# Kernel tuning notes

Hardware: AMD Instinct MI355X
Metric: run time of the kernel (lower is better)

The kernel has to match this reference:

```python
import jax, jax.numpy as jnp
import numpy as np

GROUP, BS, CH = 16, 8192, 256


def setup_inputs() -> dict:
    key = jax.random.key(0)
    kx, kw = jax.random.split(key)
    x = jax.random.normal(kx, (GROUP, BS, CH), dtype=jnp.float32)
    # PyTorch init: uniform(-stdv, stdv), stdv = 1/sqrt(channels)
    stdv = 1.0 / np.sqrt(CH)
    weight = jax.random.uniform(kw, (GROUP, CH, CH), dtype=jnp.float32,
                                minval=-stdv, maxval=stdv)
    return {"x": x, "weight": weight}


def reference(x, weight):
    # x: (group, bs, n); weight: (group, n, channels). For each column i of
    # weight (w: (group, n)) apply Householder-style reflection sequentially:
    #   x <- x - (2 / (w^T w)) * (x @ w) w^T
    ws = jnp.moveaxis(weight, -1, 0)  # (channels, group, n)

    def step(xc, w):
        denom = jnp.sum(w * w, axis=-1)              # (group,)
        xw = jnp.einsum('gbn,gn->gb', xc, w)         # (group, bs)
        xc = xc - (2.0 / denom)[:, None, None] * xw[..., None] * w[:, None, :]
        return xc, None

    out, _ = jax.lax.scan(step, x, ws)
    return out
```

## Files before the change

### kernel.cpp

```cpp
#include <hip/hip_runtime.h>
#include <hip/hip_bf16.h>

#define GROUPS 16
#define BSZ    8192
#define CHN    256

using f32x4  = __attribute__((ext_vector_type(4))) float;
using bf16x8 = __attribute__((ext_vector_type(8))) __bf16;

static __device__ __forceinline__ unsigned short f32_bf16(float f) {
    unsigned int u = __builtin_bit_cast(unsigned int, f);
    u = (u + 0x7FFFu + ((u >> 16) & 1u)) >> 16;
    return (unsigned short)u;
}
static __device__ __forceinline__ unsigned int pack_bf16x2(float lo, float hi) {
    return (unsigned int)f32_bf16(lo) | ((unsigned int)f32_bf16(hi) << 16);
}

__global__ __launch_bounds__(256) void compose_m(const float* __restrict__ weight,
                                                 unsigned short* __restrict__ Mt) {
    __shared__ float wbuf[16 * 260];
    __shared__ float coefbuf[16];

    const int t    = threadIdx.x;
    const int g    = blockIdx.x >> 4;
    const int r0   = (blockIdx.x & 15) * 16;
    const int lane = t & 15;
    const int rg   = (t >> 4) & 3;
    const int wave = t >> 6;
    const int r    = r0 + wave * 4 + rg;

    float4 m4[4];
#pragma unroll
    for (int j = 0; j < 4; ++j) {
        const int cb = 4 * lane + 64 * j;
        m4[j].x = (cb + 0 == r) ? 1.0f : 0.0f;
        m4[j].y = (cb + 1 == r) ? 1.0f : 0.0f;
        m4[j].z = (cb + 2 == r) ? 1.0f : 0.0f;
        m4[j].w = (cb + 3 == r) ? 1.0f : 0.0f;
    }

    const float* wg = weight + (size_t)g * CHN * CHN;
    const int e16 = t & 15;
    const int nb  = t >> 4;

    for (int iw = 0; iw < 16; ++iw) {
        const int i0 = iw * 16;
        float ld[16];
#pragma unroll
        for (int k = 0; k < 16; ++k)
            ld[k] = wg[(nb + 16 * k) * CHN + i0 + e16];
        __syncthreads();
#pragma unroll
        for (int k = 0; k < 16; ++k)
            wbuf[e16 * 260 + nb + 16 * k] = ld[k];
        __syncthreads();
        {
            const int e = t >> 4;
            float s = 0.0f;
#pragma unroll
            for (int k = 0; k < 16; ++k) {
                const float w = wbuf[e * 260 + lane + 16 * k];
                s += w * w;
            }
            s += __shfl_xor(s, 1);
            s += __shfl_xor(s, 2);
            s += __shfl_xor(s, 4);
            s += __shfl_xor(s, 8);
            if (lane == 0) coefbuf[e] = 2.0f / s;
        }
        __syncthreads();
#pragma unroll
        for (int e = 0; e < 16; ++e) {
            float4 w4[4];
#pragma unroll
            for (int j = 0; j < 4; ++j)
                w4[j] = *(const float4*)&wbuf[e * 260 + 4 * lane + 64 * j];
            float p = 0.0f;
#pragma unroll
            for (int j = 0; j < 4; ++j)
                p += m4[j].x * w4[j].x + m4[j].y * w4[j].y +
                     m4[j].z * w4[j].z + m4[j].w * w4[j].w;
            p += __shfl_xor(p, 1);
            p += __shfl_xor(p, 2);
            p += __shfl_xor(p, 4);
            p += __shfl_xor(p, 8);
            const float s = coefbuf[e] * p;
#pragma unroll
            for (int j = 0; j < 4; ++j) {
                m4[j].x -= s * w4[j].x;
                m4[j].y -= s * w4[j].y;
                m4[j].z -= s * w4[j].z;
                m4[j].w -= s * w4[j].w;
            }
        }
    }

    unsigned short* mg = Mt + (size_t)g * CHN * CHN;
#pragma unroll
    for (int j = 0; j < 4; ++j) {
        const int cb = 4 * lane + 64 * j;
        mg[(size_t)(cb + 0) * CHN + r] = f32_bf16(m4[j].x);
        mg[(size_t)(cb + 1) * CHN + r] = f32_bf16(m4[j].y);
        mg[(size_t)(cb + 2) * CHN + r] = f32_bf16(m4[j].z);
        mg[(size_t)(cb + 3) * CHN + r] = f32_bf16(m4[j].w);
    }
}

__global__ __launch_bounds__(512, 4) void gemm_xm(const float* __restrict__ x,
                                                  const unsigned short* __restrict__ Mt,
                                                  float* __restrict__ out) {
    __shared__ unsigned int xa [128 * 37];
    __shared__ unsigned int mts[256 * 37];

    const int t    = threadIdx.x;
    const int g    = blockIdx.x >> 6;
    const int rb   = blockIdx.x & 63;
    const int r0   = rb * 128;
    const int l    = t & 63;
    const int wave = t >> 6;
    const int wr   = wave >> 2;
    const int wc   = wave & 3;
    const int lm   = l & 15;
    const int q    = l >> 4;

    const float*          xg = x  + ((size_t)g * BSZ + r0) * CHN;
    const unsigned short* mg = Mt +  (size_t)g * CHN * CHN;

    f32x4 acc[4][4];
#pragma unroll
    for (int mi = 0; mi < 4; ++mi)
#pragma unroll
        for (int ni = 0; ni < 4; ++ni)
            acc[mi][ni] = (f32x4){0.f, 0.f, 0.f, 0.f};

    const int srr = t >> 4;
    const int sk4 = t & 15;
    const int mc  = t >> 1;
    const int mh  = t & 1;

    for (int kc = 0; kc < 4; ++kc) {
        const int k0 = kc * 64;
        __syncthreads();
#pragma unroll
        for (int it = 0; it < 4; ++it) {
            const int rr = srr + it * 32;
            const float4 v = *(const float4*)&xg[(size_t)rr * CHN + k0 + 4 * sk4];
            xa[rr * 37 + 2 * sk4 + 0] = pack_bf16x2(v.x, v.y);
            xa[rr * 37 + 2 * sk4 + 1] = pack_bf16x2(v.z, v.w);
        }
        {
            const uint4* src = (const uint4*)(mg + (size_t)mc * CHN + k0 + 32 * mh);
#pragma unroll
            for (int s = 0; s < 4; ++s) {
                const uint4 v = src[s];
                const int base = mc * 37 + 16 * mh + 4 * s;
                mts[base + 0] = v.x;
                mts[base + 1] = v.y;
                mts[base + 2] = v.z;
                mts[base + 3] = v.w;
            }
        }
        __syncthreads();
#pragma unroll
        for (int ks = 0; ks < 2; ++ks) {
            const int koff = 16 * ks + 4 * q;
            bf16x8 a[4], b[4];
#pragma unroll
            for (int mi = 0; mi < 4; ++mi) {
                const int rr = wr * 64 + mi * 16 + lm;
                uint4 u;
                u.x = xa[rr * 37 + koff + 0];
                u.y = xa[rr * 37 + koff + 1];
                u.z = xa[rr * 37 + koff + 2];
                u.w = xa[rr * 37 + koff + 3];
                a[mi] = __builtin_bit_cast(bf16x8, u);
            }
#pragma unroll
            for (int ni = 0; ni < 4; ++ni) {
                const int cc = wc * 64 + ni * 16 + lm;
                uint4 u;
                u.x = mts[cc * 37 + koff + 0];
                u.y = mts[cc * 37 + koff + 1];
                u.z = mts[cc * 37 + koff + 2];
                u.w = mts[cc * 37 + koff + 3];
                b[ni] = __builtin_bit_cast(bf16x8, u);
            }
#pragma unroll
            for (int mi = 0; mi < 4; ++mi)
#pragma unroll
                for (int ni = 0; ni < 4; ++ni)
                    acc[mi][ni] = __builtin_amdgcn_mfma_f32_16x16x32_bf16(
                        a[mi], b[ni], acc[mi][ni], 0, 0, 0);
        }
    }

    float* og = out + ((size_t)g * BSZ + r0) * CHN;
#pragma unroll
    for (int mi = 0; mi < 4; ++mi) {
#pragma unroll
        for (int ni = 0; ni < 4; ++ni) {
            const int col = wc * 64 + ni * 16 + lm;
#pragma unroll
            for (int reg = 0; reg < 4; ++reg) {
                const int row = wr * 64 + mi * 16 + q * 4 + reg;
                og[(size_t)row * CHN + col] = acc[mi][ni][reg];
            }
        }
    }
}

extern "C" void kernel_launch(void* const* d_in, const int* in_sizes, int n_in,
                              void* d_out, int out_size, void* d_ws, size_t ws_size,
                              hipStream_t stream) {
    const float* x = (const float*)d_in[0];
    const float* w = (const float*)d_in[1];
    float* out = (float*)d_out;
    unsigned short* Mt = (unsigned short*)d_ws;

    hipLaunchKernelGGL(compose_m, dim3(GROUPS * 16), dim3(256), 0, stream, w, Mt);
    hipLaunchKernelGGL(gemm_xm,   dim3(GROUPS * 64), dim3(512), 0, stream, x, Mt, out);
}
```

Measured before the change: 330.5 us.

## Replace LDS-tiled GEMM with register-streaming MFMA kernel and prefetch weights in compose

The GEMM kernel drops shared-memory staging and barriers. Each wave now owns 32 rows by all 256 columns and loads x and M fragments directly from global memory into MFMA operand registers. The compose kernel also prefetches the next weight chunk into registers before the reflection loop, and splits the dot-product reduction into four partial sums. The costs are heavy register pressure from 32 accumulators plus 16 B fragments, and redundant global reads of M across waves that now depend on the cache.

```diff
diff --git a/kernel.cpp b/kernel.cpp
--- a/kernel.cpp
+++ b/kernel.cpp
@@ -15,6 +15,14 @@
 }
 static __device__ __forceinline__ unsigned int pack_bf16x2(float lo, float hi) {
     return (unsigned int)f32_bf16(lo) | ((unsigned int)f32_bf16(hi) << 16);
+}
+static __device__ __forceinline__ bf16x8 pack8(float4 u, float4 v) {
+    uint4 d;
+    d.x = pack_bf16x2(u.x, u.y);
+    d.y = pack_bf16x2(u.z, u.w);
+    d.z = pack_bf16x2(v.x, v.y);
+    d.w = pack_bf16x2(v.z, v.w);
+    return __builtin_bit_cast(bf16x8, d);
 }
 
 __global__ __launch_bounds__(256) void compose_m(const float* __restrict__ weight,
@@ -44,17 +52,23 @@
     const int e16 = t & 15;
     const int nb  = t >> 4;
 
+    float ld[16];
+#pragma unroll
+    for (int k = 0; k < 16; ++k)
+        ld[k] = wg[(nb + 16 * k) * CHN + e16];
+
     for (int iw = 0; iw < 16; ++iw) {
-        const int i0 = iw * 16;
-        float ld[16];
-#pragma unroll
-        for (int k = 0; k < 16; ++k)
-            ld[k] = wg[(nb + 16 * k) * CHN + i0 + e16];
         __syncthreads();
 #pragma unroll
         for (int k = 0; k < 16; ++k)
             wbuf[e16 * 260 + nb + 16 * k] = ld[k];
         __syncthreads();
+        if (iw < 15) {
+            const int i0 = (iw + 1) * 16;
+#pragma unroll
+            for (int k = 0; k < 16; ++k)
+                ld[k] = wg[(nb + 16 * k) * CHN + i0 + e16];
+        }
         {
             const int e = t >> 4;
             float s = 0.0f;
@@ -76,11 +90,15 @@
 #pragma unroll
             for (int j = 0; j < 4; ++j)
                 w4[j] = *(const float4*)&wbuf[e * 260 + 4 * lane + 64 * j];
-            float p = 0.0f;
-#pragma unroll
-            for (int j = 0; j < 4; ++j)
-                p += m4[j].x * w4[j].x + m4[j].y * w4[j].y +
-                     m4[j].z * w4[j].z + m4[j].w * w4[j].w;
+            float p0 = m4[0].x * w4[0].x + m4[0].y * w4[0].y +
+                       m4[0].z * w4[0].z + m4[0].w * w4[0].w;
+            float p1 = m4[1].x * w4[1].x + m4[1].y * w4[1].y +
+                       m4[1].z * w4[1].z + m4[1].w * w4[1].w;
+            float p2 = m4[2].x * w4[2].x + m4[2].y * w4[2].y +
+                       m4[2].z * w4[2].z + m4[2].w * w4[2].w;
+            float p3 = m4[3].x * w4[3].x + m4[3].y * w4[3].y +
+                       m4[3].z * w4[3].z + m4[3].w * w4[3].w;
+            float p = (p0 + p1) + (p2 + p3);
             p += __shfl_xor(p, 1);
             p += __shfl_xor(p, 2);
             p += __shfl_xor(p, 4);
@@ -107,103 +125,62 @@
     }
 }
 
-__global__ __launch_bounds__(512, 4) void gemm_xm(const float* __restrict__ x,
-                                                  const unsigned short* __restrict__ Mt,
-                                                  float* __restrict__ out) {
-    __shared__ unsigned int xa [128 * 37];
-    __shared__ unsigned int mts[256 * 37];
-
+__global__ __launch_bounds__(256, 2) void gemm_stream(const float* __restrict__ x,
+                                                      const unsigned short* __restrict__ Mt,
+                                                      float* __restrict__ out) {
     const int t    = threadIdx.x;
+    const int wave = t >> 6;
+    const int l    = t & 63;
+    const int lm   = l & 15;
+    const int q    = l >> 4;
     const int g    = blockIdx.x >> 6;
     const int rb   = blockIdx.x & 63;
-    const int r0   = rb * 128;
-    const int l    = t & 63;
-    const int wave = t >> 6;
-    const int wr   = wave >> 2;
-    const int wc   = wave & 3;
-    const int lm   = l & 15;
-    const int q    = l >> 4;
+    const int r0   = rb * 128 + wave * 32;
 
     const float*          xg = x  + ((size_t)g * BSZ + r0) * CHN;
     const unsigned short* mg = Mt +  (size_t)g * CHN * CHN;
 
-    f32x4 acc[4][4];
-#pragma unroll
-    for (int mi = 0; mi < 4; ++mi)
-#pragma unroll
-        for (int ni = 0; ni < 4; ++ni)
+    f32x4 acc[2][16];
+#pragma unroll
+    for (int mi = 0; mi < 2; ++mi)
+#pragma unroll
+        for (int ni = 0; ni < 16; ++ni)
             acc[mi][ni] = (f32x4){0.f, 0.f, 0.f, 0.f};
 
-    const int srr = t >> 4;
-    const int sk4 = t & 15;
-    const int mc  = t >> 1;
-    const int mh  = t & 1;
-
-    for (int kc = 0; kc < 4; ++kc) {
-        const int k0 = kc * 64;
-        __syncthreads();
-#pragma unroll
-        for (int it = 0; it < 4; ++it) {
-            const int rr = srr + it * 32;
-            const float4 v = *(const float4*)&xg[(size_t)rr * CHN + k0 + 4 * sk4];
-            xa[rr * 37 + 2 * sk4 + 0] = pack_bf16x2(v.x, v.y);
-            xa[rr * 37 + 2 * sk4 + 1] = pack_bf16x2(v.z, v.w);
-        }
-        {
-            const uint4* src = (const uint4*)(mg + (size_t)mc * CHN + k0 + 32 * mh);
-#pragma unroll
-            for (int s = 0; s < 4; ++s) {
-                const uint4 v = src[s];
-                const int base = mc * 37 + 16 * mh + 4 * s;
-                mts[base + 0] = v.x;
-                mts[base + 1] = v.y;
-                mts[base + 2] = v.z;
-                mts[base + 3] = v.w;
-            }
-        }
-        __syncthreads();
-#pragma unroll
-        for (int ks = 0; ks < 2; ++ks) {
-            const int koff = 16 * ks + 4 * q;
-            bf16x8 a[4], b[4];
-#pragma unroll
-            for (int mi = 0; mi < 4; ++mi) {
-                const int rr = wr * 64 + mi * 16 + lm;
-                uint4 u;
-                u.x = xa[rr * 37 + koff + 0];
-                u.y = xa[rr * 37 + koff + 1];
-                u.z = xa[rr * 37 + koff + 2];
-                u.w = xa[rr * 37 + koff + 3];
-                a[mi] = __builtin_bit_cast(bf16x8, u);
-            }
-#pragma unroll
-            for (int ni = 0; ni < 4; ++ni) {
-                const int cc = wc * 64 + ni * 16 + lm;
-                uint4 u;
-                u.x = mts[cc * 37 + koff + 0];
-                u.y = mts[cc * 37 + koff + 1];
-                u.z = mts[cc * 37 + koff + 2];
-                u.w = mts[cc * 37 + koff + 3];
-                b[ni] = __builtin_bit_cast(bf16x8, u);
-            }
-#pragma unroll
-            for (int mi = 0; mi < 4; ++mi)
-#pragma unroll
-                for (int ni = 0; ni < 4; ++ni)
-                    acc[mi][ni] = __builtin_amdgcn_mfma_f32_16x16x32_bf16(
-                        a[mi], b[ni], acc[mi][ni], 0, 0, 0);
+    const float*          xa0 = xg + (size_t)(lm)      * CHN + q * 8;
+    const float*          xa1 = xg + (size_t)(16 + lm) * CHN + q * 8;
+    const unsigned short* mb  = mg + (size_t)lm * CHN + q * 8;
+
+    for (int kc = 0; kc < 8; ++kc) {
+        const int k0 = kc * 32;
+        const float4 a00 = *(const float4*)(xa0 + k0);
+        const float4 a01 = *(const float4*)(xa0 + k0 + 4);
+        const float4 a10 = *(const float4*)(xa1 + k0);
+        const float4 a11 = *(const float4*)(xa1 + k0 + 4);
+        uint4 bv[16];
+#pragma unroll
+        for (int ni = 0; ni < 16; ++ni)
+            bv[ni] = *(const uint4*)(mb + (size_t)ni * 16 * CHN + k0);
+
+        const bf16x8 a0 = pack8(a00, a01);
+        const bf16x8 a1 = pack8(a10, a11);
+#pragma unroll
+        for (int ni = 0; ni < 16; ++ni) {
+            const bf16x8 b = __builtin_bit_cast(bf16x8, bv[ni]);
+            acc[0][ni] = __builtin_amdgcn_mfma_f32_16x16x32_bf16(a0, b, acc[0][ni], 0, 0, 0);
+            acc[1][ni] = __builtin_amdgcn_mfma_f32_16x16x32_bf16(a1, b, acc[1][ni], 0, 0, 0);
         }
     }
 
     float* og = out + ((size_t)g * BSZ + r0) * CHN;
 #pragma unroll
-    for (int mi = 0; mi < 4; ++mi) {
-#pragma unroll
-        for (int ni = 0; ni < 4; ++ni) {
-            const int col = wc * 64 + ni * 16 + lm;
+    for (int mi = 0; mi < 2; ++mi) {
+#pragma unroll
+        for (int ni = 0; ni < 16; ++ni) {
+            const int col = ni * 16 + lm;
 #pragma unroll
             for (int reg = 0; reg < 4; ++reg) {
-                const int row = wr * 64 + mi * 16 + q * 4 + reg;
+                const int row = mi * 16 + q * 4 + reg;
                 og[(size_t)row * CHN + col] = acc[mi][ni][reg];
             }
         }
@@ -218,6 +195,6 @@
     float* out = (float*)d_out;
     unsigned short* Mt = (unsigned short*)d_ws;
 
-    hipLaunchKernelGGL(compose_m, dim3(GROUPS * 16), dim3(256), 0, stream, w, Mt);
-    hipLaunchKernelGGL(gemm_xm,   dim3(GROUPS * 64), dim3(512), 0, stream, x, Mt, out);
-}
+    hipLaunchKernelGGL(compose_m,   dim3(GROUPS * 16), dim3(256), 0, stream, w, Mt);
+    hipLaunchKernelGGL(gemm_stream, dim3(GROUPS * 64), dim3(256), 0, stream, x, Mt, out);
+}
```

Result: slower. 353.1 us (+6.8%).
